# Optimization experiments

Hardware: AMD Instinct MI355X
Metric: run time of the kernel (lower is better)

The kernel has to match this reference:

```python
import jax, jax.numpy as jnp
import numpy as np

MIN_NORM = 1e-15
BALL_EPS = 4e-3   # float32 boundary eps (HGCN PoincareBall convention)
ATANH_EPS = 1e-7  # artanh clamp margin safe in fp32 (orig 1e-15 in fp64)
C = 1.0           # curvature


def _norm(x):
    return jnp.clip(jnp.linalg.norm(x, axis=-1, keepdims=True), MIN_NORM, None)


def artanh(x):
    x = jnp.clip(x, -1.0 + ATANH_EPS, 1.0 - ATANH_EPS)
    return 0.5 * (jnp.log1p(x) - jnp.log1p(-x))


def proj(x, c):
    norm = _norm(x)
    maxnorm = (1.0 - BALL_EPS) / jnp.sqrt(c)
    return jnp.where(norm > maxnorm, x / norm * maxnorm, x)


def expmap0(u, c):
    sqrt_c = jnp.sqrt(c)
    u_norm = _norm(u)
    return jnp.tanh(sqrt_c * u_norm) * u / (sqrt_c * u_norm)


def logmap0(p, c):
    sqrt_c = jnp.sqrt(c)
    p_norm = _norm(p)
    return artanh(sqrt_c * p_norm) * p / (sqrt_c * p_norm)


def mobius_add(x, y, c):
    x2 = jnp.sum(x * x, axis=-1, keepdims=True)
    y2 = jnp.sum(y * y, axis=-1, keepdims=True)
    xy = jnp.sum(x * y, axis=-1, keepdims=True)
    num = (1.0 + 2.0 * c * xy + c * y2) * x + (1.0 - c * x2) * y
    denom = 1.0 + 2.0 * c * xy + c * c * x2 * y2
    return num / jnp.clip(denom, MIN_NORM, None)


def mobius_matvec(W, x, c):
    # W: [out, in], x: [N, in]
    sqrt_c = jnp.sqrt(c)
    x_norm = _norm(x)
    mx = x @ W.T                      # [N, out]
    mx_norm = _norm(mx)
    res_c = jnp.tanh(mx_norm / x_norm * artanh(sqrt_c * x_norm)) * mx / (mx_norm * sqrt_c)
    cond = jnp.all(mx == 0.0, axis=-1, keepdims=True)
    return jnp.where(cond, 0.0, res_c)


def setup_inputs() -> dict:
    key = jax.random.key(0)
    k1, k2 = jax.random.split(key)
    N, din, dout = 524288, 128, 128
    # points on the Poincare ball: expmap0 of small tangent vectors
    u = 0.1 * jax.random.normal(k1, (N, din), dtype=jnp.float32)
    x = proj(expmap0(u, C), C)
    # xavier_uniform with gain=sqrt(2)
    bound = np.sqrt(2.0) * np.sqrt(6.0 / (din + dout))
    W = jax.random.uniform(k2, (dout, din), dtype=jnp.float32, minval=-bound, maxval=bound)
    b = jnp.zeros((dout,), dtype=jnp.float32)
    return {"x": x, "W": W, "b": b}


def reference(x, W, b):
    # dropout p=0 / eval -> identity on W
    res = proj(mobius_matvec(W, x, C), C)
    # proj_tan0 is identity on the Poincare ball
    hyp_bias = proj(expmap0(b[None, :], C), C)
    res = proj(mobius_add(res, hyp_bias, C), C)
    # nonlinearity in tangent space at origin
    res = jax.nn.relu(logmap0(res, C))
    res = proj(expmap0(res, C), C)
    return res
```

## Files before the change

### kernel.cpp

```cpp
#include <hip/hip_runtime.h>

typedef __attribute__((ext_vector_type(8))) short short8;
typedef __attribute__((ext_vector_type(4))) float f32x4;
typedef __attribute__((ext_vector_type(4))) unsigned int u32x4;

#define MAXNORM 0.996f
#define MINNORM 1e-15f
#define ATEPS   (1.0f - 1e-7f)

__device__ __forceinline__ float frcp(float x) { return __builtin_amdgcn_rcpf(x); }
__device__ __forceinline__ float artanh_c(float z) {
    z = fminf(z, ATEPS);
    return 0.5f * __logf((1.0f + z) * frcp(1.0f - z));
}
__device__ __forceinline__ float tanh_pos(float a) {
    float e = __expf(-2.0f * a);
    return (1.0f - e) * frcp(1.0f + e);
}
__device__ __forceinline__ unsigned short f2bf(float f) {
    union { float f; unsigned u; } v; v.f = f;
    unsigned r = v.u + 0x7FFFu + ((v.u >> 16) & 1u);
    return (unsigned short)(r >> 16);
}
__device__ __forceinline__ unsigned cvt_pk_bf16(float lo, float hi) {
    unsigned r;
    asm("v_cvt_pk_bf16_f32 %0, %1, %2" : "=v"(r) : "v"(lo), "v"(hi));
    return r;
}

__global__ __launch_bounds__(256) void wpack_kernel(
    const float* __restrict__ Wf, short8* __restrict__ Wp)
{
    const int tid = blockIdx.x * 256 + threadIdx.x;
    const int l = tid & 63;
    const int f = tid >> 6;
    const int nt = f >> 2, ks = f & 3;
    const int c = l & 15, q = l >> 4;
    const float* src = Wf + (nt * 16 + c) * 128 + ks * 32 + q * 8;
    short8 s;
    #pragma unroll
    for (int j = 0; j < 4; ++j) {
        s[j]     = (short)f2bf(src[j]);
        s[4 + j] = (short)f2bf(src[4 + j]);
    }
    Wp[tid] = s;
}

__global__ __launch_bounds__(256) void blinear_kernel(
    const float* __restrict__ Xf,
    const short8* __restrict__ Wp,
    const float* __restrict__ Bf,
    float* __restrict__ Out)
{
    const int lane = threadIdx.x & 63;
    const int wave = threadIdx.x >> 6;
    const int c = lane & 15;
    const int q = lane >> 4;
    const long rowbase = (long)blockIdx.x * 128 + wave * 32;

    float b0 = Bf[lane];
    float b1 = Bf[64 + lane];
    float bn2 = b0 * b0 + b1 * b1;
    #pragma unroll
    for (int m = 1; m <= 32; m <<= 1) bn2 += __shfl_xor(bn2, m);
    float bn = fmaxf(sqrtf(bn2), MINNORM);
    float tb = tanh_pos(bn);
    float fb = fminf(tb, MAXNORM) * frcp(bn);
    float hb2 = fb * fb * bn2;
    float hbv[8];
    #pragma unroll
    for (int nt = 0; nt < 8; ++nt) hbv[nt] = fb * Bf[nt * 16 + c];

    short8 afr[2][4];
    float xq[2] = {0.0f, 0.0f};
    #pragma unroll
    for (int t = 0; t < 2; ++t) {
        const float* xrow = Xf + (rowbase + t * 16 + c) * 128;
        #pragma unroll
        for (int ks = 0; ks < 4; ++ks) {
            f32x4 a0 = *(const f32x4*)(xrow + ks * 32 + q * 8);
            f32x4 a1 = *(const f32x4*)(xrow + ks * 32 + q * 8 + 4);
            #pragma unroll
            for (int j = 0; j < 4; ++j)
                xq[t] = fmaf(a0[j], a0[j], fmaf(a1[j], a1[j], xq[t]));
            union { u32x4 u; short8 s; } cv;
            cv.u[0] = cvt_pk_bf16(a0[0], a0[1]);
            cv.u[1] = cvt_pk_bf16(a0[2], a0[3]);
            cv.u[2] = cvt_pk_bf16(a1[0], a1[1]);
            cv.u[3] = cvt_pk_bf16(a1[2], a1[3]);
            afr[t][ks] = cv.s;
        }
    }
    #pragma unroll
    for (int t = 0; t < 2; ++t) { xq[t] += __shfl_xor(xq[t], 16); xq[t] += __shfl_xor(xq[t], 32); }
    float xn2v[2][4];
    #pragma unroll
    for (int t = 0; t < 2; ++t)
        #pragma unroll
        for (int r = 0; r < 4; ++r) xn2v[t][r] = __shfl(xq[t], q * 4 + r);

    f32x4 acc[2][8];
    {
        f32x4 z = {0.0f, 0.0f, 0.0f, 0.0f};
        #pragma unroll
        for (int t = 0; t < 2; ++t)
            #pragma unroll
            for (int nt = 0; nt < 8; ++nt) acc[t][nt] = z;
    }
    #pragma unroll
    for (int nt = 0; nt < 8; ++nt) {
        #pragma unroll
        for (int ks = 0; ks < 4; ++ks) {
            short8 bfr = Wp[(nt * 4 + ks) * 64 + lane];
            acc[0][nt] = __builtin_amdgcn_mfma_f32_16x16x32_bf16(afr[0][ks], bfr, acc[0][nt], 0, 0, 0);
            acc[1][nt] = __builtin_amdgcn_mfma_f32_16x16x32_bf16(afr[1][ks], bfr, acc[1][nt], 0, 0, 0);
        }
    }

    float mn2[2][4] = {}, mhb[2][4] = {};
    #pragma unroll
    for (int t = 0; t < 2; ++t)
        #pragma unroll
        for (int nt = 0; nt < 8; ++nt)
            #pragma unroll
            for (int r = 0; r < 4; ++r) {
                float v = acc[t][nt][r];
                mn2[t][r] = fmaf(v, v, mn2[t][r]);
            }
    #pragma unroll
    for (int m = 1; m <= 8; m <<= 1)
        #pragma unroll
        for (int t = 0; t < 2; ++t)
            #pragma unroll
            for (int r = 0; r < 4; ++r) mn2[t][r] += __shfl_xor(mn2[t][r], m);
    if (hb2 != 0.0f) {
        #pragma unroll
        for (int t = 0; t < 2; ++t)
            #pragma unroll
            for (int nt = 0; nt < 8; ++nt)
                #pragma unroll
                for (int r = 0; r < 4; ++r)
                    mhb[t][r] = fmaf(acc[t][nt][r], hbv[nt], mhb[t][r]);
        #pragma unroll
        for (int m = 1; m <= 8; m <<= 1)
            #pragma unroll
            for (int t = 0; t < 2; ++t)
                #pragma unroll
                for (int r = 0; r < 4; ++r) mhb[t][r] += __shfl_xor(mhb[t][r], m);
    }

    float A1[2][4], B1[2][4], SG[2][4];
    #pragma unroll
    for (int t = 0; t < 2; ++t)
        #pragma unroll
        for (int r = 0; r < 4; ++r) {
            float xn = fmaxf(sqrtf(xn2v[t][r]), MINNORM);
            float mn = fmaxf(sqrtf(mn2[t][r]), MINNORM);
            float t1 = tanh_pos(mn * frcp(xn) * artanh_c(xn));
            float rn = fminf(t1, MAXNORM);
            float f1 = rn * frcp(mn);
            float x2 = rn * rn;
            float xy = f1 * mhb[t][r];
            float Aa = 1.0f + 2.0f * xy + hb2;
            float Bb = 1.0f - x2;
            float Dn = fmaxf(1.0f + 2.0f * xy + x2 * hb2, MINNORM);
            float rD = frcp(Dn);
            float a1 = Aa * f1 * rD;
            float b1_ = Bb * rD;
            float r2n2 = a1 * a1 * mn2[t][r] + 2.0f * a1 * b1_ * mhb[t][r] + b1_ * b1_ * hb2;
            float r2n = sqrtf(fmaxf(r2n2, 0.0f));
            float g = (r2n > MAXNORM) ? (MAXNORM * frcp(r2n)) : 1.0f;
            float n3 = fmaxf(fminf(r2n, MAXNORM), MINNORM);
            float s3 = artanh_c(n3) * frcp(n3);
            A1[t][r] = a1; B1[t][r] = b1_; SG[t][r] = s3 * g;
        }

    float q2[2][4] = {};
    if (hb2 != 0.0f) {
        #pragma unroll
        for (int t = 0; t < 2; ++t)
            #pragma unroll
            for (int nt = 0; nt < 8; ++nt)
                #pragma unroll
                for (int r = 0; r < 4; ++r) {
                    float v = fmaf(A1[t][r], acc[t][nt][r], B1[t][r] * hbv[nt]);
                    v = fmaxf(v, 0.0f);
                    acc[t][nt][r] = v;
                    q2[t][r] = fmaf(v, v, q2[t][r]);
                }
    } else {
        #pragma unroll
        for (int t = 0; t < 2; ++t)
            #pragma unroll
            for (int nt = 0; nt < 8; ++nt)
                #pragma unroll
                for (int r = 0; r < 4; ++r) {
                    float v = fmaxf(A1[t][r] * acc[t][nt][r], 0.0f);
                    acc[t][nt][r] = v;
                    q2[t][r] = fmaf(v, v, q2[t][r]);
                }
    }
    #pragma unroll
    for (int m = 1; m <= 8; m <<= 1)
        #pragma unroll
        for (int t = 0; t < 2; ++t)
            #pragma unroll
            for (int r = 0; r < 4; ++r) q2[t][r] += __shfl_xor(q2[t][r], m);

    float K[2][4];
    #pragma unroll
    for (int t = 0; t < 2; ++t)
        #pragma unroll
        for (int r = 0; r < 4; ++r) {
            float sg = SG[t][r];
            float tn_t = sg * sqrtf(q2[t][r]);
            float tn = fmaxf(tn_t, MINNORM);
            float t4 = tanh_pos(tn);
            K[t][r] = fminf(t4, MAXNORM) * frcp(tn) * sg;
        }

    #pragma unroll
    for (int t = 0; t < 2; ++t)
        #pragma unroll
        for (int r = 0; r < 4; ++r) {
            long row = rowbase + t * 16 + q * 4 + r;
            float* orow = Out + row * 128;
            #pragma unroll
            for (int nt = 0; nt < 8; ++nt)
                orow[nt * 16 + c] = K[t][r] * acc[t][nt][r];
        }
}

extern "C" void kernel_launch(void* const* d_in, const int* in_sizes, int n_in,
                              void* d_out, int out_size, void* d_ws, size_t ws_size,
                              hipStream_t stream) {
    const float* X = (const float*)d_in[0];
    const float* W = (const float*)d_in[1];
    const float* B = (const float*)d_in[2];
    float* Out = (float*)d_out;
    short8* Wp = (short8*)d_ws;
    const int N = in_sizes[0] / 128;
    wpack_kernel<<<8, 256, 0, stream>>>(W, Wp);
    blinear_kernel<<<N / 128, 256, 0, stream>>>(X, Wp, B, Out);
}
```

Before: 449.9 us.

## Swap MFMA operands so each lane holds one row for vectorized stores

Swaps the A and B operands of the MFMA so the accumulator is transposed. Each lane now holds four consecutive output columns of a single row. Row reductions shrink to two cross-lane shuffles per row instead of four-step butterflies over four rows, and the per-row scalar epilogue runs once per lane rather than four times. Output is written with 16-byte vector stores instead of scalar strided stores. The zero-bias path also folds the A1 scale into the final factor, since relu commutes with a positive scale.

```diff
diff --git a/kernel.cpp b/kernel.cpp
--- a/kernel.cpp
+++ b/kernel.cpp
@@ -64,12 +64,8 @@
     #pragma unroll
     for (int m = 1; m <= 32; m <<= 1) bn2 += __shfl_xor(bn2, m);
     float bn = fmaxf(sqrtf(bn2), MINNORM);
-    float tb = tanh_pos(bn);
-    float fb = fminf(tb, MAXNORM) * frcp(bn);
+    float fb = fminf(tanh_pos(bn), MAXNORM) * frcp(bn);
     float hb2 = fb * fb * bn2;
-    float hbv[8];
-    #pragma unroll
-    for (int nt = 0; nt < 8; ++nt) hbv[nt] = fb * Bf[nt * 16 + c];
 
     short8 afr[2][4];
     float xq[2] = {0.0f, 0.0f};
@@ -93,11 +89,6 @@
     }
     #pragma unroll
     for (int t = 0; t < 2; ++t) { xq[t] += __shfl_xor(xq[t], 16); xq[t] += __shfl_xor(xq[t], 32); }
-    float xn2v[2][4];
-    #pragma unroll
-    for (int t = 0; t < 2; ++t)
-        #pragma unroll
-        for (int r = 0; r < 4; ++r) xn2v[t][r] = __shfl(xq[t], q * 4 + r);
 
     f32x4 acc[2][8];
     {
@@ -105,130 +96,125 @@
         #pragma unroll
         for (int t = 0; t < 2; ++t)
             #pragma unroll
-            for (int nt = 0; nt < 8; ++nt) acc[t][nt] = z;
-    }
-    #pragma unroll
-    for (int nt = 0; nt < 8; ++nt) {
+            for (int mt = 0; mt < 8; ++mt) acc[t][mt] = z;
+    }
+    #pragma unroll
+    for (int mt = 0; mt < 8; ++mt) {
         #pragma unroll
         for (int ks = 0; ks < 4; ++ks) {
-            short8 bfr = Wp[(nt * 4 + ks) * 64 + lane];
-            acc[0][nt] = __builtin_amdgcn_mfma_f32_16x16x32_bf16(afr[0][ks], bfr, acc[0][nt], 0, 0, 0);
-            acc[1][nt] = __builtin_amdgcn_mfma_f32_16x16x32_bf16(afr[1][ks], bfr, acc[1][nt], 0, 0, 0);
-        }
-    }
-
-    float mn2[2][4] = {}, mhb[2][4] = {};
-    #pragma unroll
-    for (int t = 0; t < 2; ++t)
-        #pragma unroll
-        for (int nt = 0; nt < 8; ++nt)
-            #pragma unroll
-            for (int r = 0; r < 4; ++r) {
-                float v = acc[t][nt][r];
-                mn2[t][r] = fmaf(v, v, mn2[t][r]);
-            }
-    #pragma unroll
-    for (int m = 1; m <= 8; m <<= 1)
-        #pragma unroll
-        for (int t = 0; t < 2; ++t)
-            #pragma unroll
-            for (int r = 0; r < 4; ++r) mn2[t][r] += __shfl_xor(mn2[t][r], m);
+            short8 bfr = Wp[(mt * 4 + ks) * 64 + lane];
+            acc[0][mt] = __builtin_amdgcn_mfma_f32_16x16x32_bf16(bfr, afr[0][ks], acc[0][mt], 0, 0, 0);
+            acc[1][mt] = __builtin_amdgcn_mfma_f32_16x16x32_bf16(bfr, afr[1][ks], acc[1][mt], 0, 0, 0);
+        }
+    }
+
+    float mn2[2], mhb[2] = {0.0f, 0.0f};
+    #pragma unroll
+    for (int t = 0; t < 2; ++t) {
+        float s0 = 0.0f, s1 = 0.0f;
+        #pragma unroll
+        for (int mt = 0; mt < 8; ++mt) {
+            s0 = fmaf(acc[t][mt][0], acc[t][mt][0], fmaf(acc[t][mt][1], acc[t][mt][1], s0));
+            s1 = fmaf(acc[t][mt][2], acc[t][mt][2], fmaf(acc[t][mt][3], acc[t][mt][3], s1));
+        }
+        mn2[t] = s0 + s1;
+    }
+    #pragma unroll
+    for (int t = 0; t < 2; ++t) { mn2[t] += __shfl_xor(mn2[t], 16); mn2[t] += __shfl_xor(mn2[t], 32); }
     if (hb2 != 0.0f) {
         #pragma unroll
-        for (int t = 0; t < 2; ++t)
-            #pragma unroll
-            for (int nt = 0; nt < 8; ++nt)
+        for (int mt = 0; mt < 8; ++mt) {
+            f32x4 bb = *(const f32x4*)(Bf + mt * 16 + q * 4);
+            #pragma unroll
+            for (int t = 0; t < 2; ++t)
                 #pragma unroll
                 for (int r = 0; r < 4; ++r)
-                    mhb[t][r] = fmaf(acc[t][nt][r], hbv[nt], mhb[t][r]);
-        #pragma unroll
-        for (int m = 1; m <= 8; m <<= 1)
+                    mhb[t] = fmaf(acc[t][mt][r], fb * bb[r], mhb[t]);
+        }
+        #pragma unroll
+        for (int t = 0; t < 2; ++t) { mhb[t] += __shfl_xor(mhb[t], 16); mhb[t] += __shfl_xor(mhb[t], 32); }
+    }
+
+    float A1[2], B1[2], SG[2];
+    #pragma unroll
+    for (int t = 0; t < 2; ++t) {
+        float xn = fmaxf(sqrtf(xq[t]), MINNORM);
+        float mn = fmaxf(sqrtf(mn2[t]), MINNORM);
+        float t1 = tanh_pos(mn * frcp(xn) * artanh_c(xn));
+        float rn = fminf(t1, MAXNORM);
+        float f1 = rn * frcp(mn);
+        float x2 = rn * rn;
+        float xy = f1 * mhb[t];
+        float Aa = 1.0f + 2.0f * xy + hb2;
+        float Bb = 1.0f - x2;
+        float Dn = fmaxf(1.0f + 2.0f * xy + x2 * hb2, MINNORM);
+        float rD = frcp(Dn);
+        float a1 = Aa * f1 * rD;
+        float b1_ = Bb * rD;
+        float r2n2 = a1 * a1 * mn2[t] + 2.0f * a1 * b1_ * mhb[t] + b1_ * b1_ * hb2;
+        float r2n = sqrtf(fmaxf(r2n2, 0.0f));
+        float g = (r2n > MAXNORM) ? (MAXNORM * frcp(r2n)) : 1.0f;
+        float n3 = fmaxf(fminf(r2n, MAXNORM), MINNORM);
+        float s3 = artanh_c(n3) * frcp(n3);
+        A1[t] = a1; B1[t] = b1_; SG[t] = s3 * g;
+    }
+
+    float q2[2] = {0.0f, 0.0f};
+    float sA[2];
+    if (hb2 != 0.0f) {
+        #pragma unroll
+        for (int mt = 0; mt < 8; ++mt) {
+            f32x4 bb = *(const f32x4*)(Bf + mt * 16 + q * 4);
             #pragma unroll
             for (int t = 0; t < 2; ++t)
                 #pragma unroll
-                for (int r = 0; r < 4; ++r) mhb[t][r] += __shfl_xor(mhb[t][r], m);
-    }
-
-    float A1[2][4], B1[2][4], SG[2][4];
-    #pragma unroll
-    for (int t = 0; t < 2; ++t)
-        #pragma unroll
-        for (int r = 0; r < 4; ++r) {
-            float xn = fmaxf(sqrtf(xn2v[t][r]), MINNORM);
-            float mn = fmaxf(sqrtf(mn2[t][r]), MINNORM);
-            float t1 = tanh_pos(mn * frcp(xn) * artanh_c(xn));
-            float rn = fminf(t1, MAXNORM);
-            float f1 = rn * frcp(mn);
-            float x2 = rn * rn;
-            float xy = f1 * mhb[t][r];
-            float Aa = 1.0f + 2.0f * xy + hb2;
-            float Bb = 1.0f - x2;
-            float Dn = fmaxf(1.0f + 2.0f * xy + x2 * hb2, MINNORM);
-            float rD = frcp(Dn);
-            float a1 = Aa * f1 * rD;
-            float b1_ = Bb * rD;
-            float r2n2 = a1 * a1 * mn2[t][r] + 2.0f * a1 * b1_ * mhb[t][r] + b1_ * b1_ * hb2;
-            float r2n = sqrtf(fmaxf(r2n2, 0.0f));
-            float g = (r2n > MAXNORM) ? (MAXNORM * frcp(r2n)) : 1.0f;
-            float n3 = fmaxf(fminf(r2n, MAXNORM), MINNORM);
-            float s3 = artanh_c(n3) * frcp(n3);
-            A1[t][r] = a1; B1[t][r] = b1_; SG[t][r] = s3 * g;
-        }
-
-    float q2[2][4] = {};
-    if (hb2 != 0.0f) {
-        #pragma unroll
-        for (int t = 0; t < 2; ++t)
-            #pragma unroll
-            for (int nt = 0; nt < 8; ++nt)
+                for (int r = 0; r < 4; ++r) {
+                    float v = fmaf(A1[t], acc[t][mt][r], B1[t] * (fb * bb[r]));
+                    v = fmaxf(v, 0.0f);
+                    acc[t][mt][r] = v;
+                    q2[t] = fmaf(v, v, q2[t]);
+                }
+        }
+        sA[0] = 1.0f; sA[1] = 1.0f;
+    } else {
+        #pragma unroll
+        for (int t = 0; t < 2; ++t) {
+            float s0 = 0.0f, s1 = 0.0f;
+            #pragma unroll
+            for (int mt = 0; mt < 8; ++mt) {
                 #pragma unroll
-                for (int r = 0; r < 4; ++r) {
-                    float v = fmaf(A1[t][r], acc[t][nt][r], B1[t][r] * hbv[nt]);
-                    v = fmaxf(v, 0.0f);
-                    acc[t][nt][r] = v;
-                    q2[t][r] = fmaf(v, v, q2[t][r]);
-                }
-    } else {
-        #pragma unroll
-        for (int t = 0; t < 2; ++t)
-            #pragma unroll
-            for (int nt = 0; nt < 8; ++nt)
-                #pragma unroll
-                for (int r = 0; r < 4; ++r) {
-                    float v = fmaxf(A1[t][r] * acc[t][nt][r], 0.0f);
-                    acc[t][nt][r] = v;
-                    q2[t][r] = fmaf(v, v, q2[t][r]);
-                }
-    }
-    #pragma unroll
-    for (int m = 1; m <= 8; m <<= 1)
-        #pragma unroll
-        for (int t = 0; t < 2; ++t)
-            #pragma unroll
-            for (int r = 0; r < 4; ++r) q2[t][r] += __shfl_xor(q2[t][r], m);
-
-    float K[2][4];
-    #pragma unroll
-    for (int t = 0; t < 2; ++t)
-        #pragma unroll
-        for (int r = 0; r < 4; ++r) {
-            float sg = SG[t][r];
-            float tn_t = sg * sqrtf(q2[t][r]);
-            float tn = fmaxf(tn_t, MINNORM);
-            float t4 = tanh_pos(tn);
-            K[t][r] = fminf(t4, MAXNORM) * frcp(tn) * sg;
-        }
-
-    #pragma unroll
-    for (int t = 0; t < 2; ++t)
-        #pragma unroll
-        for (int r = 0; r < 4; ++r) {
-            long row = rowbase + t * 16 + q * 4 + r;
-            float* orow = Out + row * 128;
-            #pragma unroll
-            for (int nt = 0; nt < 8; ++nt)
-                orow[nt * 16 + c] = K[t][r] * acc[t][nt][r];
-        }
+                for (int r = 0; r < 4; ++r) acc[t][mt][r] = fmaxf(acc[t][mt][r], 0.0f);
+                s0 = fmaf(acc[t][mt][0], acc[t][mt][0], fmaf(acc[t][mt][1], acc[t][mt][1], s0));
+                s1 = fmaf(acc[t][mt][2], acc[t][mt][2], fmaf(acc[t][mt][3], acc[t][mt][3], s1));
+            }
+            q2[t] = s0 + s1;
+            sA[t] = A1[t];
+        }
+    }
+    #pragma unroll
+    for (int t = 0; t < 2; ++t) { q2[t] += __shfl_xor(q2[t], 16); q2[t] += __shfl_xor(q2[t], 32); }
+
+    float OS[2];
+    #pragma unroll
+    for (int t = 0; t < 2; ++t) {
+        float sgs = SG[t] * sA[t];
+        float tn_t = sgs * sqrtf(q2[t]);
+        float tn = fmaxf(tn_t, MINNORM);
+        float t4 = tanh_pos(tn);
+        OS[t] = fminf(t4, MAXNORM) * frcp(tn) * sgs;
+    }
+
+    #pragma unroll
+    for (int t = 0; t < 2; ++t) {
+        float* orow = Out + (rowbase + t * 16 + c) * 128 + q * 4;
+        #pragma unroll
+        for (int mt = 0; mt < 8; ++mt) {
+            f32x4 o;
+            #pragma unroll
+            for (int r = 0; r < 4; ++r) o[r] = OS[t] * acc[t][mt][r];
+            *(f32x4*)(orow + mt * 16) = o;
+        }
+    }
 }
 
 extern "C" void kernel_launch(void* const* d_in, const int* in_sizes, int n_in,
```

New measurement: 449.9 us. No clear change (-0.0%).
